# Kernel tuning notes

Hardware: AMD Instinct MI355X
Metric: run time of the kernel (lower is better)

## Reference

```python
import jax, jax.numpy as jnp
import numpy as np

ROPE_THETA = 10000.0

def rope(x):
    # RoPE over the FULL model_dim (applied pre head-split, as in the source),
    # interleaved even/odd pairs. x: [B, S, D]
    B, S, D = x.shape
    half = D // 2
    inv_freq = 1.0 / (ROPE_THETA ** (jnp.arange(half, dtype=jnp.float32) * 2.0 / D))
    ang = jnp.arange(S, dtype=jnp.float32)[:, None] * inv_freq[None, :]  # [S, half]
    cos, sin = jnp.cos(ang), jnp.sin(ang)
    x1, x2 = x[..., 0::2], x[..., 1::2]
    r1 = x1 * cos - x2 * sin
    r2 = x1 * sin + x2 * cos
    return jnp.stack([r1, r2], axis=-1).reshape(B, S, D)


def setup_inputs() -> dict:
    key = jax.random.key(0)
    ks = jax.random.split(key, 9)
    B, S, D = 4, 2048, 768
    w = 0.02
    return {
        "X":  jax.random.normal(ks[0], (B, S, D), dtype=jnp.float32),
        "Wq": jax.random.normal(ks[1], (D, D), dtype=jnp.float32) * w,
        "bq": jnp.zeros((D,), dtype=jnp.float32),
        "Wk": jax.random.normal(ks[2], (D, D), dtype=jnp.float32) * w,
        "bk": jnp.zeros((D,), dtype=jnp.float32),
        "Wv": jax.random.normal(ks[3], (D, D), dtype=jnp.float32) * w,
        "bv": jnp.zeros((D,), dtype=jnp.float32),
        "Wo": jax.random.normal(ks[4], (D, D), dtype=jnp.float32) * w,
        "bo": jnp.zeros((D,), dtype=jnp.float32),
    }


def reference(X, Wq, bq, Wk, bk, Wv, bv, Wo, bo):
    NUM_HEADS = 12
    B, S, D = X.shape
    hd = D // NUM_HEADS

    q = rope(X @ Wq + bq)   # RoPE applied pre-split on full model_dim
    k = rope(X @ Wk + bk)
    v = X @ Wv + bv

    # Contiguous per-head slices == reshape to [B, S, H, hd]
    qh = q.reshape(B, S, NUM_HEADS, hd)
    kh = k.reshape(B, S, NUM_HEADS, hd)
    vh = v.reshape(B, S, NUM_HEADS, hd)

    scores = jnp.einsum('bqhd,bkhd->bhqk', qh, kh) / jnp.sqrt(jnp.float32(hd))
    causal = jnp.tril(jnp.ones((S, S), dtype=bool))
    scores = jnp.where(causal[None, None, :, :], scores, -jnp.inf)
    weights = jax.nn.softmax(scores, axis=-1)
    out = jnp.einsum('bhqk,bkhd->bqhd', weights, vh).reshape(B, S, D)
    return out @ Wo + bo
```

## Files before the change

### kernel.cpp

```cpp
#include <hip/hip_runtime.h>
#include <math.h>

#define D_MODEL 768
#define NUM_HEADS 12
#define HEAD_DIM 64
#define SEQ 2048
#define BATCH 4
#define MROWS (BATCH * SEQ)
#define HALF_D (D_MODEL / 2)

typedef __bf16    bf16x8 __attribute__((ext_vector_type(8)));
typedef _Float16  f16x4  __attribute__((ext_vector_type(4)));
typedef float     f32x4  __attribute__((ext_vector_type(4)));

__device__ __forceinline__ void gload_lds16(const void* gp, void* lp) {
    __builtin_amdgcn_global_load_lds(
        (const __attribute__((address_space(1))) unsigned int*)gp,
        (__attribute__((address_space(3))) unsigned int*)lp, 16, 0, 0);
}

__global__ __launch_bounds__(256)
void prep(const float* __restrict__ X, __bf16* __restrict__ Xb,
          const float* __restrict__ W0, const float* __restrict__ W1,
          const float* __restrict__ W2, const float* __restrict__ W3,
          __bf16* __restrict__ T0, __bf16* __restrict__ T1,
          __bf16* __restrict__ T2, __bf16* __restrict__ T3)
{
    __shared__ float t[64][65];
    const int n   = blockIdx.x;
    const int tid = threadIdx.x;

    if (n < 3072) {
        size_t i = ((size_t)n * 256 + tid) * 8;
        float4 u = *(const float4*)(X + i);
        float4 v = *(const float4*)(X + i + 4);
        bf16x8 o;
        o[0]=(__bf16)u.x; o[1]=(__bf16)u.y; o[2]=(__bf16)u.z; o[3]=(__bf16)u.w;
        o[4]=(__bf16)v.x; o[5]=(__bf16)v.y; o[6]=(__bf16)v.z; o[7]=(__bf16)v.w;
        *(bf16x8*)(Xb + i) = o;
    } else {
        int m = n - 3072;
        int z = m / 144;
        int rem = m - z * 144;
        int by = rem / 12, bx = rem % 12;
        const float* W = z == 0 ? W0 : z == 1 ? W1 : z == 2 ? W2 : W3;
        __bf16*      T = z == 0 ? T0 : z == 1 ? T1 : z == 2 ? T2 : T3;

        const int r0 = by * 64, c0 = bx * 64;
        const int lx = tid & 63, g = tid >> 6;

        #pragma unroll
        for (int rr = 0; rr < 16; ++rr) {
            int r = g * 16 + rr;
            t[r][lx] = W[(size_t)(r0 + r) * D_MODEL + c0 + lx];
        }
        __syncthreads();

        const int nn = tid >> 2;
        const int kb = (tid & 3) * 16;
        bf16x8 o1, o2;
        #pragma unroll
        for (int mm = 0; mm < 8; ++mm) o1[mm] = (__bf16)t[kb + mm][nn];
        #pragma unroll
        for (int mm = 0; mm < 8; ++mm) o2[mm] = (__bf16)t[kb + 8 + mm][nn];
        __bf16* dst = T + (size_t)(c0 + nn) * D_MODEL + r0 + kb;
        *(bf16x8*)dst       = o1;
        *(bf16x8*)(dst + 8) = o2;
    }
}

__global__ __launch_bounds__(512, 2)
void qkv_gemm(const __bf16* __restrict__ Xb,
              const __bf16* __restrict__ Wqt, const __bf16* __restrict__ Wkt,
              const __bf16* __restrict__ Wvt,
              const float* __restrict__ bq, const float* __restrict__ bk,
              const float* __restrict__ bv,
              __bf16* __restrict__ Qb, __bf16* __restrict__ Kb,
              _Float16* __restrict__ Vtb)
{
    __shared__ bf16x8 Asf[3][16][64];
    __shared__ bf16x8 Bsf[3][16][64];

    const int tid  = threadIdx.x;
    const int wv   = tid >> 6;
    const int ln   = tid & 63;
    const int t15  = ln & 15;
    const int quad = ln >> 4;
    const int wr = wv >> 2, wc = wv & 3;

    const int lin = blockIdx.x;
    const int c   = lin >> 5;
    const int r   = lin & 31;
    const int which = c / 3;
    const int col0  = (c % 3) * 256;
    const int row0  = r * 256;

    const __bf16* Wt  = which == 0 ? Wqt : which == 1 ? Wkt : Wvt;
    const float* bias = which == 0 ? bq  : which == 1 ? bk  : bv;

    f32x4 acc[8][4];
    #pragma unroll
    for (int i = 0; i < 8; ++i)
        #pragma unroll
        for (int j = 0; j < 4; ++j) acc[i][j] = (f32x4){0.f,0.f,0.f,0.f};

    const __bf16* seg[4];
    bf16x8*       dstp[4];
    #pragma unroll
    for (int u = 0; u < 4; ++u) {
        const int id   = wv * 4 + u;
        const int isB  = id >> 4;
        const int slot = id & 15;
        const __bf16* base = isB
            ? Wt + (size_t)(col0 + 16 * slot + t15) * D_MODEL
            : Xb + (size_t)(row0 + 16 * slot + t15) * D_MODEL;
        seg[u]  = base + 8 * quad;
        dstp[u] = isB ? &Bsf[0][slot][0] : &Asf[0][slot][0];
    }

    auto stage_all = [&](int buf, int k0) {
        #pragma unroll
        for (int u = 0; u < 4; ++u)
            gload_lds16(seg[u] + k0, dstp[u] + buf * 1024);
    };

    stage_all(0, 0);
    stage_all(1, 32);

    const int NT = D_MODEL / 32;
    int cur = 0, nx = 2;
    for (int t = 0; t < NT; ++t) {
        if (t < NT - 1) { asm volatile("s_waitcnt vmcnt(4)" ::: "memory"); }
        else            { asm volatile("s_waitcnt vmcnt(0)" ::: "memory"); }
        __builtin_amdgcn_s_barrier();
        const bool doStage = (t + 2 < NT);
        const int  kS      = 32 * (t + 2);

        #pragma unroll
        for (int p = 0; p < 4; ++p) {
            if (doStage)
                gload_lds16(seg[p] + kS, dstp[p] + nx * 1024);

            const int rh = p >> 1, ch = p & 1;
            bf16x8 af[4], bfr[2];
            #pragma unroll
            for (int i = 0; i < 4; ++i) af[i]  = Asf[cur][8 * wr + 4 * rh + i][ln];
            #pragma unroll
            for (int j = 0; j < 2; ++j) bfr[j] = Bsf[cur][4 * wc + 2 * ch + j][ln];

            __builtin_amdgcn_s_setprio(1);
            #pragma unroll
            for (int i = 0; i < 4; ++i)
                #pragma unroll
                for (int j = 0; j < 2; ++j)
                    acc[4 * rh + i][2 * ch + j] =
                        __builtin_amdgcn_mfma_f32_16x16x32_bf16(af[i], bfr[j],
                            acc[4 * rh + i][2 * ch + j], 0, 0, 0);
            __builtin_amdgcn_s_setprio(0);
            __builtin_amdgcn_s_barrier();
        }

        cur = (cur == 2) ? 0 : cur + 1;
        nx  = (nx  == 2) ? 0 : nx  + 1;
    }

    if (which < 2) {
        const float oscale = (which == 0) ? 0.125f : 1.0f;
        __bf16* dstq = which ? Kb : Qb;
        #pragma unroll
        for (int i = 0; i < 8; ++i) {
            const int rowb = row0 + 128 * wr + 16 * i + 4 * quad;
            const int s0   = rowb & (SEQ - 1);
            #pragma unroll
            for (int j = 0; j < 4; ++j) {
                const int col = col0 + 64 * wc + 16 * j + t15;
                const float bval = bias[col];
                const int ne = col & ~1;
                const float fr = __expf((float)ne * (-9.210340371976184f / 768.0f));
                const float cf = __cosf(fr), sf = __sinf(fr);
                const float sgn = (col & 1) ? 1.0f : -1.0f;
                float ang = (float)s0 * fr;
                float ca = __cosf(ang), sa = __sinf(ang);
                #pragma unroll
                for (int rr = 0; rr < 4; ++rr) {
                    const int rw = rowb + rr;
                    float val  = acc[i][j][rr] + bval;
                    float part = __shfl_xor(val, 1, 64);
                    dstq[(size_t)rw * D_MODEL + col] = (__bf16)((val * ca + part * sgn * sa) * oscale);
                    float cn = ca * cf - sa * sf;
                    sa = sa * cf + ca * sf;
                    ca = cn;
                }
            }
        }
    } else {
        #pragma unroll
        for (int i = 0; i < 8; ++i) {
            const int rowb = row0 + 128 * wr + 16 * i + 4 * quad;
            #pragma unroll
            for (int j = 0; j < 4; ++j) {
                const int col = col0 + 64 * wc + 16 * j + t15;
                const float bval = bias[col];
                const int h = col >> 6, d = col & 63;
                const int bidx = rowb >> 11, s = rowb & (SEQ - 1);
                f16x4 pk;
                #pragma unroll
                for (int rr = 0; rr < 4; ++rr) pk[rr] = (_Float16)(acc[i][j][rr] + bval);
                *(f16x4*)(Vtb + ((size_t)(bidx * NUM_HEADS + h) * 64 + d) * SEQ + s) = pk;
            }
        }
    }
}

__global__ __launch_bounds__(512, 2)
void out_gemm(const __bf16* __restrict__ Ab, const __bf16* __restrict__ Wt,
              const float* __restrict__ bias, float* __restrict__ Cout)
{
    __shared__ bf16x8 Asf[3][8][64];
    __shared__ bf16x8 Bsf[3][12][64];

    const int tid  = threadIdx.x;
    const int wv   = tid >> 6;
    const int ln   = tid & 63;
    const int t15  = ln & 15;
    const int quad = ln >> 4;
    const int wr = wv >> 2, wc = wv & 3;

    const int lin  = blockIdx.x;
    const int col0 = (lin >> 6) * 192;
    const int row0 = (lin & 63) * 128;

    f32x4 acc[4][3];
    #pragma unroll
    for (int i = 0; i < 4; ++i)
        #pragma unroll
        for (int j = 0; j < 3; ++j) acc[i][j] = (f32x4){0.f,0.f,0.f,0.f};

    const int base = (wv < 4) ? wv * 3 : 12 + (wv - 4) * 2;
    const int nseg = (wv < 4) ? 3 : 2;
    const __bf16* seg[3];
    bf16x8*       dstp[3];
    int           bstr[3];
    #pragma unroll
    for (int u = 0; u < 3; ++u) {
        const int id   = base + ((u < nseg) ? u : 0);
        const int isB  = id >= 8;
        const int slot = isB ? id - 8 : id;
        const __bf16* bb = isB
            ? Wt + (size_t)(col0 + 16 * slot + t15) * D_MODEL
            : Ab + (size_t)(row0 + 16 * slot + t15) * D_MODEL;
        seg[u]  = bb + 8 * quad;
        dstp[u] = isB ? &Bsf[0][slot][0] : &Asf[0][slot][0];
        bstr[u] = isB ? 12 * 64 : 8 * 64;
    }

    auto stage = [&](int buf, int k0) {
        #pragma unroll
        for (int u = 0; u < 3; ++u)
            if (u < nseg)
                gload_lds16(seg[u] + k0, dstp[u] + buf * bstr[u]);
    };

    stage(0, 0);
    stage(1, 32);

    const int NT = D_MODEL / 32;
    int cur = 0, nx = 2;
    for (int t = 0; t < NT; ++t) {
        if (t < NT - 1) {
            if (wv < 4) { asm volatile("s_waitcnt vmcnt(3)" ::: "memory"); }
            else        { asm volatile("s_waitcnt vmcnt(2)" ::: "memory"); }
        } else          { asm volatile("s_waitcnt vmcnt(0)" ::: "memory"); }
        __builtin_amdgcn_s_barrier();
        if (t + 2 < NT) stage(nx, 32 * (t + 2));

        bf16x8 af[4], bfr[3];
        #pragma unroll
        for (int i = 0; i < 4; ++i) af[i]  = Asf[cur][4 * wr + i][ln];
        #pragma unroll
        for (int j = 0; j < 3; ++j) bfr[j] = Bsf[cur][3 * wc + j][ln];
        #pragma unroll
        for (int i = 0; i < 4; ++i)
            #pragma unroll
            for (int j = 0; j < 3; ++j)
                acc[i][j] = __builtin_amdgcn_mfma_f32_16x16x32_bf16(af[i], bfr[j], acc[i][j], 0, 0, 0);

        cur = (cur == 2) ? 0 : cur + 1;
        nx  = (nx  == 2) ? 0 : nx  + 1;
    }

    #pragma unroll
    for (int i = 0; i < 4; ++i) {
        const int rowb = row0 + 64 * wr + 16 * i + 4 * quad;
        #pragma unroll
        for (int j = 0; j < 3; ++j) {
            const int col = col0 + 48 * wc + 16 * j + t15;
            const float bval = bias[col];
            #pragma unroll
            for (int rr = 0; rr < 4; ++rr)
                Cout[(size_t)(rowb + rr) * D_MODEL + col] = acc[i][j][rr] + bval;
        }
    }
}

__device__ __forceinline__ void attn_tile(
    const bf16x8 (*Kbuf)[64], const _Float16* Vbuf ,
    bf16x8 aq0, bf16x8 aq1,
    f32x4* o, float& lacc,
    int ln, int t15, int quad, int j0, int qglob, bool domask)
{
    f32x4 s[4];
    #pragma unroll
    for (int c = 0; c < 4; ++c) {
        s[c] = (f32x4){0.f, 0.f, 0.f, 0.f};
        s[c] = __builtin_amdgcn_mfma_f32_16x16x32_bf16(Kbuf[c][ln],     aq0, s[c], 0, 0, 0);
        s[c] = __builtin_amdgcn_mfma_f32_16x16x32_bf16(Kbuf[4 + c][ln], aq1, s[c], 0, 0, 0);
    }

    f16x4 pf[4];
    #pragma unroll
    for (int c = 0; c < 4; ++c)
        #pragma unroll
        for (int r = 0; r < 4; ++r) {
            float e = __expf(s[c][r]);
            if (domask && (j0 + 16 * c + 4 * quad + r > qglob)) e = 0.f;
            lacc += e;
            pf[c][r] = (_Float16)e;
        }

    #pragma unroll
    for (int c = 0; c < 4; ++c) {
        const int lv = 16 * (2 * (c & 1) + (quad >> 1)) + t15;
        const int jb = 4 * (quad & 1);
        #pragma unroll
        for (int cd = 0; cd < 4; ++cd) {
            f16x4 vf = *(const f16x4*)&Vbuf[(size_t)(4 * (c >> 1) + cd) * 512 + lv * 8 + jb];
            o[cd] = __builtin_amdgcn_mfma_f32_16x16x16f16(pf[c], vf, o[cd], 0, 0, 0);
        }
    }
}

__global__ __launch_bounds__(512)
void attn_flash(const __bf16* __restrict__ Q, const __bf16* __restrict__ K,
                const _Float16* __restrict__ Vt, __bf16* __restrict__ O)
{
    __shared__ bf16x8   Kf[2][8][64];
    __shared__ _Float16 Vh[2][8][512];

    const int tid  = threadIdx.x;
    const int wv   = tid >> 6;
    const int ln   = tid & 63;
    const int t15  = ln & 15;
    const int quad = ln >> 4;

    const int n  = blockIdx.x;
    const int qt = 15 - (n / 48);
    const int bh = n % 48;
    const int b  = bh / NUM_HEADS;
    const int h  = bh % NUM_HEADS;
    const int q0 = qt * 128;
    const int nt = (q0 >> 6) + 2;

    bf16x8 aq0, aq1;
    {
        const __bf16* qs = Q + (size_t)(b * SEQ + q0 + 16 * wv + t15) * D_MODEL + h * 64 + 8 * quad;
        aq0 = *(const bf16x8*)qs;
        aq1 = *(const bf16x8*)(qs + 32);
    }

    const __bf16*   kp = K  + ((size_t)b * SEQ + 16 * (wv & 3) + t15) * D_MODEL
                            + h * 64 + 32 * (wv >> 2) + 8 * quad;
    const _Float16* vp = Vt + ((size_t)bh * 64 + 16 * (wv & 3) + t15) * SEQ
                            + 32 * (wv >> 2) + 8 * quad;

    f32x4 o[4];
    #pragma unroll
    for (int c = 0; c < 4; ++c) o[c] = (f32x4){0.f,0.f,0.f,0.f};
    float lacc = 0.f;
    const int qglob = q0 + 16 * wv + t15;
    const int wmax  = q0 + 16 * wv + 15;

    gload_lds16(kp, &Kf[0][wv][0]);
    gload_lds16(vp, &Vh[0][wv][0]);

    int cur = 0;
    for (int it = 0; it < nt; ++it) {
        __syncthreads();
        if (it + 1 < nt) {
            const int jn = (it + 1) * 64;
            gload_lds16(kp + (size_t)jn * D_MODEL, &Kf[cur ^ 1][wv][0]);
            gload_lds16(vp + jn,                   &Vh[cur ^ 1][wv][0]);
        }
        const int j0 = it * 64;
        if (j0 <= wmax) {
            const bool domask = (j0 + 63) > (q0 + 16 * wv);
            attn_tile(Kf[cur], &Vh[cur][0][0], aq0, aq1, o, lacc,
                      ln, t15, quad, j0, qglob, domask);
        }
        cur ^= 1;
    }

    lacc += __shfl_xor(lacc, 16, 64);
    lacc += __shfl_xor(lacc, 32, 64);

    float inv[4];
    #pragma unroll
    for (int r = 0; r < 4; ++r)
        inv[r] = 1.0f / __shfl(lacc, 4 * quad + r, 64);

    #pragma unroll
    for (int c = 0; c < 4; ++c)
        #pragma unroll
        for (int r = 0; r < 4; ++r) {
            int row = q0 + 16 * wv + 4 * quad + r;
            O[(size_t)(b * SEQ + row) * D_MODEL + h * 64 + 16 * c + t15] = (__bf16)(o[c][r] * inv[r]);
        }
}

extern "C" void kernel_launch(void* const* d_in, const int* in_sizes, int n_in,
                              void* d_out, int out_size, void* d_ws, size_t ws_size,
                              hipStream_t stream) {
    const float* X  = (const float*)d_in[0];
    const float* Wq = (const float*)d_in[1];
    const float* bq = (const float*)d_in[2];
    const float* Wk = (const float*)d_in[3];
    const float* bk = (const float*)d_in[4];
    const float* Wv = (const float*)d_in[5];
    const float* bv = (const float*)d_in[6];
    const float* Wo = (const float*)d_in[7];
    const float* bo = (const float*)d_in[8];
    float* out = (float*)d_out;

    const size_t BSD = (size_t)MROWS * D_MODEL;
    const size_t WSZ = (size_t)D_MODEL * D_MODEL;

    __bf16*   Xb  = (__bf16*)d_ws;
    __bf16*   Qb  = Xb  + BSD;
    __bf16*   Kb  = Qb  + BSD;
    _Float16* Vtb = (_Float16*)(Kb + BSD);
    __bf16*   Ob  = (__bf16*)(Vtb + BSD);
    __bf16*   Wqt = Ob  + BSD;
    __bf16*   Wkt = Wqt + WSZ;
    __bf16*   Wvt = Wkt + WSZ;
    __bf16*   Wot = Wvt + WSZ;

    prep<<<3648, 256, 0, stream>>>(X, Xb, Wq, Wk, Wv, Wo, Wqt, Wkt, Wvt, Wot);

    qkv_gemm<<<288, 512, 0, stream>>>(Xb, Wqt, Wkt, Wvt, bq, bk, bv, Qb, Kb, Vtb);

    attn_flash<<<768, 512, 0, stream>>>(Qb, Kb, Vtb, Ob);

    out_gemm<<<256, 512, 0, stream>>>(Ob, Wot, bo, out);
}
```

Baseline: 231.3 us.

## Process two 16-row query groups per wave in attention, halving block size

Each wave in the flash attention kernel now handles 32 query rows (two 16-row groups) instead of 16. The block shrinks from 512 to 256 threads, and each thread stages two K and two V chunks per tile. Every K/V fragment read from LDS is reused across two MFMA groups, which cuts LDS traffic per FLOP. The cost is more registers per thread (doubled accumulators and scores), which may lower occupancy, and less parallelism per block.

```diff
diff --git a/kernel.cpp b/kernel.cpp
--- a/kernel.cpp
+++ b/kernel.cpp
@@ -303,44 +303,7 @@
     }
 }
 
-__device__ __forceinline__ void attn_tile(
-    const bf16x8 (*Kbuf)[64], const _Float16* Vbuf ,
-    bf16x8 aq0, bf16x8 aq1,
-    f32x4* o, float& lacc,
-    int ln, int t15, int quad, int j0, int qglob, bool domask)
-{
-    f32x4 s[4];
-    #pragma unroll
-    for (int c = 0; c < 4; ++c) {
-        s[c] = (f32x4){0.f, 0.f, 0.f, 0.f};
-        s[c] = __builtin_amdgcn_mfma_f32_16x16x32_bf16(Kbuf[c][ln],     aq0, s[c], 0, 0, 0);
-        s[c] = __builtin_amdgcn_mfma_f32_16x16x32_bf16(Kbuf[4 + c][ln], aq1, s[c], 0, 0, 0);
-    }
-
-    f16x4 pf[4];
-    #pragma unroll
-    for (int c = 0; c < 4; ++c)
-        #pragma unroll
-        for (int r = 0; r < 4; ++r) {
-            float e = __expf(s[c][r]);
-            if (domask && (j0 + 16 * c + 4 * quad + r > qglob)) e = 0.f;
-            lacc += e;
-            pf[c][r] = (_Float16)e;
-        }
-
-    #pragma unroll
-    for (int c = 0; c < 4; ++c) {
-        const int lv = 16 * (2 * (c & 1) + (quad >> 1)) + t15;
-        const int jb = 4 * (quad & 1);
-        #pragma unroll
-        for (int cd = 0; cd < 4; ++cd) {
-            f16x4 vf = *(const f16x4*)&Vbuf[(size_t)(4 * (c >> 1) + cd) * 512 + lv * 8 + jb];
-            o[cd] = __builtin_amdgcn_mfma_f32_16x16x16f16(pf[c], vf, o[cd], 0, 0, 0);
-        }
-    }
-}
-
-__global__ __launch_bounds__(512)
+__global__ __launch_bounds__(256)
 void attn_flash(const __bf16* __restrict__ Q, const __bf16* __restrict__ K,
                 const _Float16* __restrict__ Vt, __bf16* __restrict__ O)
 {
@@ -361,60 +324,130 @@
     const int q0 = qt * 128;
     const int nt = (q0 >> 6) + 2;
 
-    bf16x8 aq0, aq1;
-    {
-        const __bf16* qs = Q + (size_t)(b * SEQ + q0 + 16 * wv + t15) * D_MODEL + h * 64 + 8 * quad;
-        aq0 = *(const bf16x8*)qs;
-        aq1 = *(const bf16x8*)(qs + 32);
-    }
-
-    const __bf16*   kp = K  + ((size_t)b * SEQ + 16 * (wv & 3) + t15) * D_MODEL
-                            + h * 64 + 32 * (wv >> 2) + 8 * quad;
-    const _Float16* vp = Vt + ((size_t)bh * 64 + 16 * (wv & 3) + t15) * SEQ
-                            + 32 * (wv >> 2) + 8 * quad;
-
-    f32x4 o[4];
-    #pragma unroll
-    for (int c = 0; c < 4; ++c) o[c] = (f32x4){0.f,0.f,0.f,0.f};
-    float lacc = 0.f;
-    const int qglob = q0 + 16 * wv + t15;
-    const int wmax  = q0 + 16 * wv + 15;
-
-    gload_lds16(kp, &Kf[0][wv][0]);
-    gload_lds16(vp, &Vh[0][wv][0]);
+    bf16x8 aq0[2], aq1[2];
+    #pragma unroll
+    for (int g = 0; g < 2; ++g) {
+        const __bf16* qs = Q + (size_t)(b * SEQ + q0 + 32 * wv + 16 * g + t15) * D_MODEL
+                             + h * 64 + 8 * quad;
+        aq0[g] = *(const bf16x8*)qs;
+        aq1[g] = *(const bf16x8*)(qs + 32);
+    }
+
+    const __bf16*   kp = K  + ((size_t)b * SEQ + 16 * wv + t15) * D_MODEL
+                            + h * 64 + 8 * quad;
+    const _Float16* vp = Vt + ((size_t)bh * 64 + 16 * wv + t15) * SEQ + 8 * quad;
+
+    f32x4 o[2][4];
+    float lacc[2] = {0.f, 0.f};
+    #pragma unroll
+    for (int g = 0; g < 2; ++g)
+        #pragma unroll
+        for (int c = 0; c < 4; ++c) o[g][c] = (f32x4){0.f,0.f,0.f,0.f};
+
+    int qglob[2], gbase[2];
+    #pragma unroll
+    for (int g = 0; g < 2; ++g) {
+        gbase[g] = q0 + 32 * wv + 16 * g;
+        qglob[g] = gbase[g] + t15;
+    }
+    const int wmax1 = gbase[1] + 15;
+    const int wmax0 = gbase[0] + 15;
+
+    auto stage = [&](int buf, int it) {
+        const int jn = it * 64;
+        gload_lds16(kp + (size_t)jn * D_MODEL,      &Kf[buf][wv][0]);
+        gload_lds16(kp + (size_t)jn * D_MODEL + 32, &Kf[buf][wv + 4][0]);
+        gload_lds16(vp + jn,                        &Vh[buf][wv][0]);
+        gload_lds16(vp + jn + 32,                   &Vh[buf][wv + 4][0]);
+    };
+
+    stage(0, 0);
 
     int cur = 0;
     for (int it = 0; it < nt; ++it) {
         __syncthreads();
-        if (it + 1 < nt) {
-            const int jn = (it + 1) * 64;
-            gload_lds16(kp + (size_t)jn * D_MODEL, &Kf[cur ^ 1][wv][0]);
-            gload_lds16(vp + jn,                   &Vh[cur ^ 1][wv][0]);
-        }
+        if (it + 1 < nt) stage(cur ^ 1, it + 1);
+
         const int j0 = it * 64;
-        if (j0 <= wmax) {
-            const bool domask = (j0 + 63) > (q0 + 16 * wv);
-            attn_tile(Kf[cur], &Vh[cur][0][0], aq0, aq1, o, lacc,
-                      ln, t15, quad, j0, qglob, domask);
+        if (j0 <= wmax1) {
+            const bool act0 = (j0 <= wmax0);
+            const bool dm0  = (j0 + 63) > gbase[0];
+            const bool dm1  = (j0 + 63) > gbase[1];
+            const bf16x8   (*Kbuf)[64] = Kf[cur];
+            const _Float16* Vbuf       = &Vh[cur][0][0];
+
+            f32x4 s[2][4];
+            #pragma unroll
+            for (int c = 0; c < 4; ++c) {
+                const bf16x8 kf0 = Kbuf[c][ln];
+                const bf16x8 kf1 = Kbuf[4 + c][ln];
+                if (act0) {
+                    s[0][c] = (f32x4){0.f,0.f,0.f,0.f};
+                    s[0][c] = __builtin_amdgcn_mfma_f32_16x16x32_bf16(kf0, aq0[0], s[0][c], 0, 0, 0);
+                    s[0][c] = __builtin_amdgcn_mfma_f32_16x16x32_bf16(kf1, aq1[0], s[0][c], 0, 0, 0);
+                }
+                s[1][c] = (f32x4){0.f,0.f,0.f,0.f};
+                s[1][c] = __builtin_amdgcn_mfma_f32_16x16x32_bf16(kf0, aq0[1], s[1][c], 0, 0, 0);
+                s[1][c] = __builtin_amdgcn_mfma_f32_16x16x32_bf16(kf1, aq1[1], s[1][c], 0, 0, 0);
+            }
+
+            f16x4 pf[2][4];
+            #pragma unroll
+            for (int c = 0; c < 4; ++c) {
+                if (act0) {
+                    #pragma unroll
+                    for (int r = 0; r < 4; ++r) {
+                        float e = __expf(s[0][c][r]);
+                        if (dm0 && (j0 + 16 * c + 4 * quad + r > qglob[0])) e = 0.f;
+                        lacc[0] += e;
+                        pf[0][c][r] = (_Float16)e;
+                    }
+                }
+                #pragma unroll
+                for (int r = 0; r < 4; ++r) {
+                    float e = __expf(s[1][c][r]);
+                    if (dm1 && (j0 + 16 * c + 4 * quad + r > qglob[1])) e = 0.f;
+                    lacc[1] += e;
+                    pf[1][c][r] = (_Float16)e;
+                }
+            }
+
+            #pragma unroll
+            for (int c = 0; c < 4; ++c) {
+                const int lv = 16 * (2 * (c & 1) + (quad >> 1)) + t15;
+                const int jb = 4 * (quad & 1);
+                #pragma unroll
+                for (int cd = 0; cd < 4; ++cd) {
+                    const f16x4 vf = *(const f16x4*)&Vbuf[(size_t)(4 * (c >> 1) + cd) * 512 + lv * 8 + jb];
+                    if (act0)
+                        o[0][cd] = __builtin_amdgcn_mfma_f32_16x16x16f16(pf[0][c], vf, o[0][cd], 0, 0, 0);
+                    o[1][cd] = __builtin_amdgcn_mfma_f32_16x16x16f16(pf[1][c], vf, o[1][cd], 0, 0, 0);
+                }
+            }
         }
         cur ^= 1;
     }
 
-    lacc += __shfl_xor(lacc, 16, 64);
-    lacc += __shfl_xor(lacc, 32, 64);
-
-    float inv[4];
-    #pragma unroll
-    for (int r = 0; r < 4; ++r)
-        inv[r] = 1.0f / __shfl(lacc, 4 * quad + r, 64);
-
-    #pragma unroll
-    for (int c = 0; c < 4; ++c)
-        #pragma unroll
-        for (int r = 0; r < 4; ++r) {
-            int row = q0 + 16 * wv + 4 * quad + r;
-            O[(size_t)(b * SEQ + row) * D_MODEL + h * 64 + 16 * c + t15] = (__bf16)(o[c][r] * inv[r]);
-        }
+    #pragma unroll
+    for (int g = 0; g < 2; ++g) {
+        float la = lacc[g];
+        la += __shfl_xor(la, 16, 64);
+        la += __shfl_xor(la, 32, 64);
+
+        float inv[4];
+        #pragma unroll
+        for (int r = 0; r < 4; ++r)
+            inv[r] = 1.0f / __shfl(la, 4 * quad + r, 64);
+
+        #pragma unroll
+        for (int c = 0; c < 4; ++c)
+            #pragma unroll
+            for (int r = 0; r < 4; ++r) {
+                const int row = gbase[g] + 4 * quad + r;
+                O[(size_t)(b * SEQ + row) * D_MODEL + h * 64 + 16 * c + t15] =
+                    (__bf16)(o[g][c][r] * inv[r]);
+            }
+    }
 }
 
 extern "C" void kernel_launch(void* const* d_in, const int* in_sizes, int n_in,
@@ -448,7 +481,7 @@
 
     qkv_gemm<<<288, 512, 0, stream>>>(Xb, Wqt, Wkt, Wvt, bq, bk, bv, Qb, Kb, Vtb);
 
-    attn_flash<<<768, 512, 0, stream>>>(Qb, Kb, Vtb, Ob);
+    attn_flash<<<768, 256, 0, stream>>>(Qb, Kb, Vtb, Ob);
 
     out_gemm<<<256, 512, 0, stream>>>(Ob, Wot, bo, out);
 }
```

New measurement: 248.8 us. 1.08x slower.
